# Kernel tuning notes

Measured on AMD Instinct MI355X. Metric: run time of the kernel, lower is better.

Reference implementation:

```python
import jax, jax.numpy as jnp
import numpy as np

K_NN = 10      # knn_graph(landmarks, 10)
K_HOPS = 2     # TAGConv K
DELTA_T = 10
EPS = 0.1


def knn_edges(pos, k=K_NN):
    # PyG knn_graph with loop=False, flow='source_to_target':
    # edges (src=neighbor j, dst=query i), k nearest excluding self.
    n = pos.shape[0]
    sq = jnp.sum(pos * pos, axis=-1)
    d = sq[:, None] + sq[None, :] - 2.0 * (pos @ pos.T)  # [N,N] squared dists
    d = jnp.where(jnp.eye(n, dtype=bool), jnp.inf, d)
    _, idx = jax.lax.top_k(-d, k)                        # [N,k] neighbor ids
    src = idx.reshape(-1)                                # neighbors (sources)
    dst = jnp.repeat(jnp.arange(n), k)                   # query nodes (targets)
    return src, dst


def tagconv(h, src, dst, conv_ws, conv_b):
    # out = sum_{k=0..K} (A_norm^k h) W_k + b, gcn_norm without self-loops
    n = h.shape[0]
    deg = jax.ops.segment_sum(jnp.ones_like(src, dtype=h.dtype), dst, num_segments=n)
    dinv = jnp.where(deg > 0, jax.lax.rsqrt(deg), 0.0)
    norm = dinv[src] * dinv[dst]                         # [E]
    out = h @ conv_ws[0]
    x = h
    for k in range(1, K_HOPS + 1):
        msg = x[src] * norm[:, None]                     # gather + scale [E,D]
        x = jax.ops.segment_sum(msg, dst, num_segments=n)
        out = out + x @ conv_ws[k]
    return out + conv_b


def setup_inputs() -> dict:
    key = jax.random.key(0)
    ks = jax.random.split(key, 7)
    N, D_IN, D_H, D_OUT = 8192, 3, 256, 3
    s_emb = 1.0 / np.sqrt(D_IN)
    s_h = 1.0 / np.sqrt(D_H)
    return {
        "landmarks": jax.random.normal(ks[0], (N, D_IN), jnp.float32),
        "emb_w": jax.random.normal(ks[1], (D_IN, D_H), jnp.float32) * s_emb,
        "emb_b": jax.random.normal(ks[2], (D_H,), jnp.float32) * 0.01,
        "readout_w": jax.random.normal(ks[3], (D_H, D_OUT), jnp.float32) * s_h,
        "readout_b": jax.random.normal(ks[4], (D_OUT,), jnp.float32) * 0.01,
        "conv_ws": jax.random.normal(ks[5], (K_HOPS + 1, D_H, D_H), jnp.float32) * s_h,
        "conv_b": jax.random.normal(ks[6], (D_H,), jnp.float32) * 0.01,
    }


def reference(landmarks, emb_w, emb_b, readout_w, readout_b, conv_ws, conv_b):
    src, dst = knn_edges(landmarks)
    h = landmarks @ emb_w + emb_b                        # emb
    x = h @ readout_w + readout_b                        # readout of initial state

    def step(hc, _):
        c = tagconv(hc, src, dst, conv_ws, conv_b)
        hn = hc + EPS * jnp.tanh(c)                      # Euler residual step
        return hn, hn @ readout_w + readout_b

    h_final, land_pred = jax.lax.scan(step, h, None, length=DELTA_T)
    y = h_final @ readout_w + readout_b
    return y, h_final, x, land_pred
```

## Files before the change

### kernel.cpp

```cpp
#include <hip/hip_runtime.h>
#include <float.h>
#include <math.h>

#define NN 8192
#define DH 256
#define KNN 10
#define TSTEPS 10
#define EPSC 0.1f
#define CTILE 1024
#define QPB 16

typedef short s8v __attribute__((ext_vector_type(8)));
typedef float f4v __attribute__((ext_vector_type(4)));

__device__ __forceinline__ float bf2f(unsigned short u) {
    union { unsigned u; float f; } c; c.u = ((unsigned)u) << 16; return c.f;
}
__device__ __forceinline__ unsigned short f2bf(float f) {
    union { float f; unsigned u; } c; c.f = f;
    unsigned r = c.u + 0x7FFF + ((c.u >> 16) & 1);
    return (unsigned short)(r >> 16);
}

__global__ void prep_wt(const float* __restrict__ W, unsigned short* __restrict__ Wt) {
    int e = blockIdx.x * 256 + threadIdx.x;
    int g = e >> 16; int rem = e & 65535;
    int n = rem >> 8; int k = rem & 255;
    Wt[e] = f2bf(W[g * 65536 + k * 256 + n]);
}

__global__ void prep_pos(const float* __restrict__ pos, float4* __restrict__ pos4) {
    int j = blockIdx.x * 256 + threadIdx.x;
    float x = pos[j * 3], y = pos[j * 3 + 1], z = pos[j * 3 + 2];
    float4 v; v.x = x; v.y = y; v.z = z; v.w = x * x + y * y + z * z;
    pos4[j] = v;
}

__launch_bounds__(1024)
__global__ void knn_wave(const float* __restrict__ pos, const float4* __restrict__ pos4,
                         int* __restrict__ nbr) {
    __shared__ float4 cand[CTILE];
    int tid = threadIdx.x;
    int wv = tid >> 6, lane = tid & 63;
    int i = blockIdx.x * QPB + wv;
    float xi = pos[i * 3], yi = pos[i * 3 + 1], zi = pos[i * 3 + 2];
    float sqi = xi * xi + yi * yi + zi * zi;
    int igrp = i & ~63;

    float b  = FLT_MAX;
    int   ib = -1;
    float thr = FLT_MAX;

    for (int tile = 0; tile < NN / CTILE; ++tile) {
        __syncthreads();
        cand[tid] = pos4[tile * CTILE + tid];
        __syncthreads();
#pragma unroll 4
        for (int u = 0; u < CTILE / 64; ++u) {
            int jgrp = tile * CTILE + u * 64;
            float4 c = cand[u * 64 + lane];
            int j = jgrp + lane;
            float m = c.x * xi + c.y * yi + c.z * zi;
            float d = (sqi + c.w) - 2.0f * m;
            if (jgrp == igrp) {
                if (j == i) d = FLT_MAX;
            }
            unsigned long long mask = __ballot(d < thr);
            while (mask) {
                int l = __ffsll((unsigned long long)mask) - 1;
                mask &= mask - 1;
                float dc = __int_as_float(__builtin_amdgcn_readlane(__float_as_int(d), l));
                if (dc < thr) {
                    int jc = __builtin_amdgcn_readlane(j, l);
                    float bp = __int_as_float(__builtin_amdgcn_update_dpp(
                        0, __float_as_int(b), 0x111, 0xF, 0xF, true));
                    int ip = __builtin_amdgcn_update_dpp(0, ib, 0x111, 0xF, 0xF, true);
                    bool c0 = dc < b;
                    bool cp = (lane != 0) && (dc < bp);
                    b  = c0 ? (cp ? bp : dc) : b;
                    ib = c0 ? (cp ? ip : jc) : ib;
                    thr = __int_as_float(__builtin_amdgcn_readlane(__float_as_int(b), 9));
                }
            }
        }
    }
    if (lane < KNN) nbr[i * KNN + lane] = ib;
}

__global__ void emb_kernel(const float* __restrict__ lm, const float* __restrict__ ew,
                           const float* __restrict__ eb, const float* __restrict__ rw,
                           const float* __restrict__ rb,
                           float* __restrict__ hdo, unsigned short* __restrict__ hbf,
                           float* __restrict__ xout) {
    __shared__ float s0[4], s1[4], s2[4];
    int i = blockIdx.x, d = threadIdx.x;
    float a0 = lm[i * 3], a1 = lm[i * 3 + 1], a2 = lm[i * 3 + 2];
    float h = eb[d] + a0 * ew[d] + a1 * ew[256 + d] + a2 * ew[512 + d];
    hdo[i * 256 + d] = h;
    hbf[i * 256 + d] = f2bf(h);
    float p0 = h * rw[d * 3], p1 = h * rw[d * 3 + 1], p2 = h * rw[d * 3 + 2];
    for (int off = 32; off; off >>= 1) {
        p0 += __shfl_down(p0, off, 64);
        p1 += __shfl_down(p1, off, 64);
        p2 += __shfl_down(p2, off, 64);
    }
    int lane = d & 63, wid = d >> 6;
    if (lane == 0) { s0[wid] = p0; s1[wid] = p1; s2[wid] = p2; }
    __syncthreads();
    if (d == 0) {
        xout[i * 3 + 0] = s0[0] + s0[1] + s0[2] + s0[3] + rb[0];
        xout[i * 3 + 1] = s1[0] + s1[1] + s1[2] + s1[3] + rb[1];
        xout[i * 3 + 2] = s2[0] + s2[1] + s2[2] + s2[3] + rb[2];
    }
}

__global__ void agg_kernel(const unsigned short* __restrict__ src,
                           unsigned short* __restrict__ dst,
                           const int* __restrict__ nbr) {
    int tid = threadIdx.x;
    int wid = tid >> 6, lane = tid & 63;
    int node = blockIdx.x * 4 + wid;
    int d0 = lane * 4;
    float a0 = 0.f, a1 = 0.f, a2 = 0.f, a3 = 0.f;
    const int* nb = nbr + node * KNN;
    for (int q = 0; q < KNN; q++) {
        int j = nb[q];
        uint2 v = *(const uint2*)(src + j * 256 + d0);
        a0 += bf2f((unsigned short)(v.x & 0xffff));
        a1 += bf2f((unsigned short)(v.x >> 16));
        a2 += bf2f((unsigned short)(v.y & 0xffff));
        a3 += bf2f((unsigned short)(v.y >> 16));
    }
    uint2 o;
    o.x = (unsigned)f2bf(a0 * 0.1f) | ((unsigned)f2bf(a1 * 0.1f) << 16);
    o.y = (unsigned)f2bf(a2 * 0.1f) | ((unsigned)f2bf(a3 * 0.1f) << 16);
    *(uint2*)(dst + node * 256 + d0) = o;
}

__launch_bounds__(1024)
__global__ void gemm_step(unsigned short* hbf,
                          const unsigned short* __restrict__ x1,
                          const int* __restrict__ nbr,
                          const unsigned short* __restrict__ Wt,
                          const float* __restrict__ cb,
                          const float* __restrict__ rw, const float* __restrict__ rb,
                          float* hdo, float* __restrict__ yout, float* yfin) {
    __shared__ __align__(16) short Al[32 * 264];
    __shared__ __align__(16) short X2[32 * 264];
    __shared__ __align__(16) short Bl[2][256 * 72];
    __shared__ float rwl[768];
    __shared__ float cbl[256];
    __shared__ float yred[16][4][4][3];

    int tid = threadIdx.x;
    int m0 = blockIdx.x * 32;
    if (tid < 768) rwl[tid] = rw[tid];
    if (tid < 256) cbl[tid] = cb[tid];

    int w = tid >> 6, lane = tid & 63;
    int quad = lane >> 4, l15 = lane & 15;
    int rt = w >> 3, cfg = w & 7;

    int arow = tid >> 5, acg = tid & 31;
    int bn = tid >> 2, bk = (tid & 3) * 16;

    {
        const int* nb = nbr + (m0 + arow) * KNN;
        float a[8];
#pragma unroll
        for (int e = 0; e < 8; e++) a[e] = 0.f;
        for (int q = 0; q < KNN; q++) {
            int j = nb[q];
            uint4 v = *(const uint4*)(x1 + j * 256 + acg * 8);
            a[0] += bf2f((unsigned short)(v.x & 0xffff));
            a[1] += bf2f((unsigned short)(v.x >> 16));
            a[2] += bf2f((unsigned short)(v.y & 0xffff));
            a[3] += bf2f((unsigned short)(v.y >> 16));
            a[4] += bf2f((unsigned short)(v.z & 0xffff));
            a[5] += bf2f((unsigned short)(v.z >> 16));
            a[6] += bf2f((unsigned short)(v.w & 0xffff));
            a[7] += bf2f((unsigned short)(v.w >> 16));
        }
        uint4 o;
        o.x = (unsigned)f2bf(a[0]*0.1f) | ((unsigned)f2bf(a[1]*0.1f) << 16);
        o.y = (unsigned)f2bf(a[2]*0.1f) | ((unsigned)f2bf(a[3]*0.1f) << 16);
        o.z = (unsigned)f2bf(a[4]*0.1f) | ((unsigned)f2bf(a[5]*0.1f) << 16);
        o.w = (unsigned)f2bf(a[6]*0.1f) | ((unsigned)f2bf(a[7]*0.1f) << 16);
        *(uint4*)((unsigned short*)&X2[arow * 264 + acg * 8]) = o;
    }

    {
        uint4 va = *(const uint4*)(((const unsigned short*)hbf) + (m0 + arow) * 256 + acg * 8);
        *(uint4*)((unsigned short*)&Al[arow * 264 + acg * 8]) = va;
        uint4 v0 = *(const uint4*)(Wt + bn * 256 + bk);
        uint4 v1 = *(const uint4*)(Wt + bn * 256 + bk + 8);
        *(uint4*)(&Bl[0][bn * 72 + bk]) = v0;
        *(uint4*)(&Bl[0][bn * 72 + bk + 8]) = v1;
    }
    __syncthreads();

    f4v acc[2];
    acc[0] = (f4v){0.f, 0.f, 0.f, 0.f};
    acc[1] = (f4v){0.f, 0.f, 0.f, 0.f};

#pragma unroll
    for (int kc = 0; kc < 12; kc++) {
        const int cur = kc & 1;
        uint4 v0, v1;
        if (kc + 1 < 12) {
            const unsigned short* bsrc = Wt + ((kc + 1) >> 2) * 65536 + ((kc + 1) & 3) * 64;
            v0 = *(const uint4*)(bsrc + bn * 256 + bk);
            v1 = *(const uint4*)(bsrc + bn * 256 + bk + 8);
        }
        uint4 va;
        if (kc == 3)
            va = *(const uint4*)(x1 + (m0 + arow) * 256 + acg * 8);
        {
            const short* Abase = (kc < 8) ? Al : X2;
            int kl = (kc & 3) * 64;
#pragma unroll
            for (int ks = 0; ks < 2; ks++) {
                s8v a = *(const s8v*)(&Abase[(rt * 16 + l15) * 264 + kl + ks * 32 + quad * 8]);
#pragma unroll
                for (int f = 0; f < 2; f++) {
                    int n = (cfg * 2 + f) * 16 + l15;
                    s8v b = *(const s8v*)(&Bl[cur][n * 72 + ks * 32 + quad * 8]);
                    acc[f] = __builtin_amdgcn_mfma_f32_16x16x32_bf16(a, b, acc[f], 0, 0, 0);
                }
            }
        }
        if (kc + 1 < 12) {
            *(uint4*)(&Bl[cur ^ 1][bn * 72 + bk]) = v0;
            *(uint4*)(&Bl[cur ^ 1][bn * 72 + bk + 8]) = v1;
        }
        __syncthreads();
        if (kc == 3) {
            *(uint4*)((unsigned short*)&Al[arow * 264 + acg * 8]) = va;
            __syncthreads();
        }
    }

    float py[4][3] = {};
#pragma unroll
    for (int f = 0; f < 2; f++) {
        int col = (cfg * 2 + f) * 16 + l15;
        float cbv = cbl[col];
        float rw0 = rwl[col * 3], rw1 = rwl[col * 3 + 1], rw2 = rwl[col * 3 + 2];
#pragma unroll
        for (int r = 0; r < 4; r++) {
            int grow = m0 + rt * 16 + quad * 4 + r;
            float cval = acc[f][r] + cbv;
            float hn = hdo[grow * 256 + col] + EPSC * tanhf(cval);
            hdo[grow * 256 + col] = hn;
            hbf[grow * 256 + col] = f2bf(hn);
            py[r][0] += hn * rw0; py[r][1] += hn * rw1; py[r][2] += hn * rw2;
        }
    }
    for (int off = 1; off < 16; off <<= 1)
        for (int r = 0; r < 4; r++)
            for (int j = 0; j < 3; j++)
                py[r][j] += __shfl_xor(py[r][j], off, 64);
    if (l15 == 0)
        for (int r = 0; r < 4; r++)
            for (int j = 0; j < 3; j++)
                yred[w][quad][r][j] = py[r][j];
    __syncthreads();
    if (w == 0 && l15 == 0) {
        for (int rt2 = 0; rt2 < 2; rt2++) {
            for (int r = 0; r < 4; r++) {
                int grow = m0 + rt2 * 16 + quad * 4 + r;
                for (int j = 0; j < 3; j++) {
                    float yv = rb[j];
                    for (int ww = rt2 * 8; ww < rt2 * 8 + 8; ww++)
                        yv += yred[ww][quad][r][j];
                    yout[grow * 3 + j] = yv;
                    if (yfin) yfin[grow * 3 + j] = yv;
                }
            }
        }
    }
}

extern "C" void kernel_launch(void* const* d_in, const int* in_sizes, int n_in,
                              void* d_out, int out_size, void* d_ws, size_t ws_size,
                              hipStream_t stream) {
    const float* lm = (const float*)d_in[0];
    const float* ew = (const float*)d_in[1];
    const float* eb = (const float*)d_in[2];
    const float* rw = (const float*)d_in[3];
    const float* rb = (const float*)d_in[4];
    const float* cw = (const float*)d_in[5];
    const float* cb = (const float*)d_in[6];

    float* out = (float*)d_out;
    float* y_out = out;
    float* h_out = out + 24576;
    float* x_out = out + 24576 + 2097152;
    float* lp_out = x_out + 24576;

    char* ws = (char*)d_ws;
    int* nbr = (int*)ws;                       ws += NN * KNN * sizeof(int);
    float4* pos4 = (float4*)ws;                ws += NN * sizeof(float4);
    char* uni = ws;
    unsigned short* hbf = (unsigned short*)uni;
    unsigned short* x1  = hbf + NN * DH;
    unsigned short* Wt  = x1 + NN * DH;

    prep_pos<<<NN / 256, 256, 0, stream>>>(lm, pos4);
    knn_wave<<<NN / QPB, 1024, 0, stream>>>(lm, pos4, nbr);
    prep_wt<<<768, 256, 0, stream>>>(cw, Wt);
    emb_kernel<<<NN, 256, 0, stream>>>(lm, ew, eb, rw, rb, h_out, hbf, x_out);
    for (int t = 0; t < TSTEPS; t++) {
        agg_kernel<<<NN / 4, 256, 0, stream>>>(hbf, x1, nbr);
        gemm_step<<<NN / 32, 1024, 0, stream>>>(hbf, x1, nbr, Wt, cb, rw, rb, h_out,
                                                lp_out + t * 24576,
                                                (t == TSTEPS - 1) ? y_out : nullptr);
    }
}
```

Before: 398.8 us.

## Pre-swizzle weights into MFMA fragment layout and drop LDS B staging

Weights are now pre-permuted on the device into the exact per-lane MFMA B-fragment order, so the GEMM reads B fragments straight from global/L2 with no LDS double buffering and no barriers inside the k-loop. The GEMM tile shrinks to 16 rows with 512 threads and a launch bound of 4 blocks per CU, trading B reuse across rows for occupancy and fewer syncs. The aggregation kernel switches to 16-byte loads with all ten neighbour loads issued up front. The main risk is higher L2 traffic for weights, since every block re-reads all 384 KB of Wt.

```diff
diff --git a/kernel.cpp b/kernel.cpp
--- a/kernel.cpp
+++ b/kernel.cpp
@@ -24,8 +24,11 @@
 
 __global__ void prep_wt(const float* __restrict__ W, unsigned short* __restrict__ Wt) {
     int e = blockIdx.x * 256 + threadIdx.x;
-    int g = e >> 16; int rem = e & 65535;
-    int n = rem >> 8; int k = rem & 255;
+    int i8 = e & 7, lane = (e >> 3) & 63, nb = (e >> 9) & 15;
+    int ks = (e >> 13) & 1, kc2 = (e >> 14) & 3, g = e >> 16;
+    int quad = lane >> 4, l15 = lane & 15;
+    int k = kc2 * 64 + ks * 32 + quad * 8 + i8;
+    int n = nb * 16 + l15;
     Wt[e] = f2bf(W[g * 65536 + k * 256 + n]);
 }
 
@@ -118,26 +121,39 @@
                            unsigned short* __restrict__ dst,
                            const int* __restrict__ nbr) {
     int tid = threadIdx.x;
-    int wid = tid >> 6, lane = tid & 63;
-    int node = blockIdx.x * 4 + wid;
-    int d0 = lane * 4;
-    float a0 = 0.f, a1 = 0.f, a2 = 0.f, a3 = 0.f;
+    int slot = tid >> 5, l32 = tid & 31;
+    int node = blockIdx.x * 8 + slot;
+    int d0 = l32 * 8;
     const int* nb = nbr + node * KNN;
+    int j[KNN];
+#pragma unroll
+    for (int q = 0; q < KNN; q++) j[q] = nb[q];
+    uint4 v[KNN];
+#pragma unroll
+    for (int q = 0; q < KNN; q++) v[q] = *(const uint4*)(src + j[q] * 256 + d0);
+    float a[8];
+#pragma unroll
+    for (int e = 0; e < 8; e++) a[e] = 0.f;
+#pragma unroll
     for (int q = 0; q < KNN; q++) {
-        int j = nb[q];
-        uint2 v = *(const uint2*)(src + j * 256 + d0);
-        a0 += bf2f((unsigned short)(v.x & 0xffff));
-        a1 += bf2f((unsigned short)(v.x >> 16));
-        a2 += bf2f((unsigned short)(v.y & 0xffff));
-        a3 += bf2f((unsigned short)(v.y >> 16));
-    }
-    uint2 o;
-    o.x = (unsigned)f2bf(a0 * 0.1f) | ((unsigned)f2bf(a1 * 0.1f) << 16);
-    o.y = (unsigned)f2bf(a2 * 0.1f) | ((unsigned)f2bf(a3 * 0.1f) << 16);
-    *(uint2*)(dst + node * 256 + d0) = o;
-}
-
-__launch_bounds__(1024)
+        a[0] += bf2f((unsigned short)(v[q].x & 0xffff));
+        a[1] += bf2f((unsigned short)(v[q].x >> 16));
+        a[2] += bf2f((unsigned short)(v[q].y & 0xffff));
+        a[3] += bf2f((unsigned short)(v[q].y >> 16));
+        a[4] += bf2f((unsigned short)(v[q].z & 0xffff));
+        a[5] += bf2f((unsigned short)(v[q].z >> 16));
+        a[6] += bf2f((unsigned short)(v[q].w & 0xffff));
+        a[7] += bf2f((unsigned short)(v[q].w >> 16));
+    }
+    uint4 o;
+    o.x = (unsigned)f2bf(a[0]*0.1f) | ((unsigned)f2bf(a[1]*0.1f) << 16);
+    o.y = (unsigned)f2bf(a[2]*0.1f) | ((unsigned)f2bf(a[3]*0.1f) << 16);
+    o.z = (unsigned)f2bf(a[4]*0.1f) | ((unsigned)f2bf(a[5]*0.1f) << 16);
+    o.w = (unsigned)f2bf(a[6]*0.1f) | ((unsigned)f2bf(a[7]*0.1f) << 16);
+    *(uint4*)(dst + node * 256 + d0) = o;
+}
+
+__launch_bounds__(512, 4)
 __global__ void gemm_step(unsigned short* hbf,
                           const unsigned short* __restrict__ x1,
                           const int* __restrict__ nbr,
@@ -145,33 +161,39 @@
                           const float* __restrict__ cb,
                           const float* __restrict__ rw, const float* __restrict__ rb,
                           float* hdo, float* __restrict__ yout, float* yfin) {
-    __shared__ __align__(16) short Al[32 * 264];
-    __shared__ __align__(16) short X2[32 * 264];
-    __shared__ __align__(16) short Bl[2][256 * 72];
+    __shared__ __align__(16) short Ah[16 * 264];
+    __shared__ __align__(16) short A1[16 * 264];
+    __shared__ __align__(16) short X2[16 * 264];
     __shared__ float rwl[768];
     __shared__ float cbl[256];
-    __shared__ float yred[16][4][4][3];
+    __shared__ float yred[8][4][4][3];
 
     int tid = threadIdx.x;
-    int m0 = blockIdx.x * 32;
-    if (tid < 768) rwl[tid] = rw[tid];
+    int m0 = blockIdx.x * 16;
+    for (int idx = tid; idx < 768; idx += 512) rwl[idx] = rw[idx];
     if (tid < 256) cbl[tid] = cb[tid];
 
     int w = tid >> 6, lane = tid & 63;
     int quad = lane >> 4, l15 = lane & 15;
-    int rt = w >> 3, cfg = w & 7;
-
-    int arow = tid >> 5, acg = tid & 31;
-    int bn = tid >> 2, bk = (tid & 3) * 16;
+    int row = tid >> 5, cg = tid & 31;
 
     {
-        const int* nb = nbr + (m0 + arow) * KNN;
+        uint4 va = *(const uint4*)(((const unsigned short*)hbf) + (m0 + row) * 256 + cg * 8);
+        *(uint4*)((unsigned short*)&Ah[row * 264 + cg * 8]) = va;
+        uint4 vb = *(const uint4*)(x1 + (m0 + row) * 256 + cg * 8);
+        *(uint4*)((unsigned short*)&A1[row * 264 + cg * 8]) = vb;
+    }
+    {
+        const int* nb = nbr + (m0 + row) * KNN;
+        int j[KNN];
+#pragma unroll
+        for (int q = 0; q < KNN; q++) j[q] = nb[q];
         float a[8];
 #pragma unroll
         for (int e = 0; e < 8; e++) a[e] = 0.f;
+#pragma unroll
         for (int q = 0; q < KNN; q++) {
-            int j = nb[q];
-            uint4 v = *(const uint4*)(x1 + j * 256 + acg * 8);
+            uint4 v = *(const uint4*)(x1 + j[q] * 256 + cg * 8);
             a[0] += bf2f((unsigned short)(v.x & 0xffff));
             a[1] += bf2f((unsigned short)(v.x >> 16));
             a[2] += bf2f((unsigned short)(v.y & 0xffff));
@@ -186,16 +208,7 @@
         o.y = (unsigned)f2bf(a[2]*0.1f) | ((unsigned)f2bf(a[3]*0.1f) << 16);
         o.z = (unsigned)f2bf(a[4]*0.1f) | ((unsigned)f2bf(a[5]*0.1f) << 16);
         o.w = (unsigned)f2bf(a[6]*0.1f) | ((unsigned)f2bf(a[7]*0.1f) << 16);
-        *(uint4*)((unsigned short*)&X2[arow * 264 + acg * 8]) = o;
-    }
-
-    {
-        uint4 va = *(const uint4*)(((const unsigned short*)hbf) + (m0 + arow) * 256 + acg * 8);
-        *(uint4*)((unsigned short*)&Al[arow * 264 + acg * 8]) = va;
-        uint4 v0 = *(const uint4*)(Wt + bn * 256 + bk);
-        uint4 v1 = *(const uint4*)(Wt + bn * 256 + bk + 8);
-        *(uint4*)(&Bl[0][bn * 72 + bk]) = v0;
-        *(uint4*)(&Bl[0][bn * 72 + bk + 8]) = v1;
+        *(uint4*)((unsigned short*)&X2[row * 264 + cg * 8]) = o;
     }
     __syncthreads();
 
@@ -205,50 +218,28 @@
 
 #pragma unroll
     for (int kc = 0; kc < 12; kc++) {
-        const int cur = kc & 1;
-        uint4 v0, v1;
-        if (kc + 1 < 12) {
-            const unsigned short* bsrc = Wt + ((kc + 1) >> 2) * 65536 + ((kc + 1) & 3) * 64;
-            v0 = *(const uint4*)(bsrc + bn * 256 + bk);
-            v1 = *(const uint4*)(bsrc + bn * 256 + bk + 8);
-        }
-        uint4 va;
-        if (kc == 3)
-            va = *(const uint4*)(x1 + (m0 + arow) * 256 + acg * 8);
-        {
-            const short* Abase = (kc < 8) ? Al : X2;
-            int kl = (kc & 3) * 64;
-#pragma unroll
-            for (int ks = 0; ks < 2; ks++) {
-                s8v a = *(const s8v*)(&Abase[(rt * 16 + l15) * 264 + kl + ks * 32 + quad * 8]);
-#pragma unroll
-                for (int f = 0; f < 2; f++) {
-                    int n = (cfg * 2 + f) * 16 + l15;
-                    s8v b = *(const s8v*)(&Bl[cur][n * 72 + ks * 32 + quad * 8]);
-                    acc[f] = __builtin_amdgcn_mfma_f32_16x16x32_bf16(a, b, acc[f], 0, 0, 0);
-                }
+        const short* Ab = (kc < 4) ? Ah : (kc < 8) ? A1 : X2;
+        int kl = (kc & 3) * 64;
+#pragma unroll
+        for (int ks = 0; ks < 2; ks++) {
+            s8v a = *(const s8v*)(&Ab[l15 * 264 + kl + ks * 32 + quad * 8]);
+#pragma unroll
+            for (int f = 0; f < 2; f++) {
+                s8v b = *(const s8v*)(Wt + ((kc * 2 + ks) * 16 + (w * 2 + f)) * 512 + lane * 8);
+                acc[f] = __builtin_amdgcn_mfma_f32_16x16x32_bf16(a, b, acc[f], 0, 0, 0);
             }
         }
-        if (kc + 1 < 12) {
-            *(uint4*)(&Bl[cur ^ 1][bn * 72 + bk]) = v0;
-            *(uint4*)(&Bl[cur ^ 1][bn * 72 + bk + 8]) = v1;
-        }
-        __syncthreads();
-        if (kc == 3) {
-            *(uint4*)((unsigned short*)&Al[arow * 264 + acg * 8]) = va;
-            __syncthreads();
-        }
     }
 
     float py[4][3] = {};
 #pragma unroll
     for (int f = 0; f < 2; f++) {
-        int col = (cfg * 2 + f) * 16 + l15;
+        int col = w * 32 + f * 16 + l15;
         float cbv = cbl[col];
         float rw0 = rwl[col * 3], rw1 = rwl[col * 3 + 1], rw2 = rwl[col * 3 + 2];
 #pragma unroll
         for (int r = 0; r < 4; r++) {
-            int grow = m0 + rt * 16 + quad * 4 + r;
+            int grow = m0 + quad * 4 + r;
             float cval = acc[f][r] + cbv;
             float hn = hdo[grow * 256 + col] + EPSC * tanhf(cval);
             hdo[grow * 256 + col] = hn;
@@ -266,16 +257,13 @@
                 yred[w][quad][r][j] = py[r][j];
     __syncthreads();
     if (w == 0 && l15 == 0) {
-        for (int rt2 = 0; rt2 < 2; rt2++) {
-            for (int r = 0; r < 4; r++) {
-                int grow = m0 + rt2 * 16 + quad * 4 + r;
-                for (int j = 0; j < 3; j++) {
-                    float yv = rb[j];
-                    for (int ww = rt2 * 8; ww < rt2 * 8 + 8; ww++)
-                        yv += yred[ww][quad][r][j];
-                    yout[grow * 3 + j] = yv;
-                    if (yfin) yfin[grow * 3 + j] = yv;
-                }
+        for (int r = 0; r < 4; r++) {
+            int grow = m0 + quad * 4 + r;
+            for (int j = 0; j < 3; j++) {
+                float yv = rb[j];
+                for (int ww = 0; ww < 8; ww++) yv += yred[ww][quad][r][j];
+                yout[grow * 3 + j] = yv;
+                if (yfin) yfin[grow * 3 + j] = yv;
             }
         }
     }
@@ -311,9 +299,9 @@
     prep_wt<<<768, 256, 0, stream>>>(cw, Wt);
     emb_kernel<<<NN, 256, 0, stream>>>(lm, ew, eb, rw, rb, h_out, hbf, x_out);
     for (int t = 0; t < TSTEPS; t++) {
-        agg_kernel<<<NN / 4, 256, 0, stream>>>(hbf, x1, nbr);
-        gemm_step<<<NN / 32, 1024, 0, stream>>>(hbf, x1, nbr, Wt, cb, rw, rb, h_out,
-                                                lp_out + t * 24576,
-                                                (t == TSTEPS - 1) ? y_out : nullptr);
-    }
-}
+        agg_kernel<<<NN / 8, 256, 0, stream>>>(hbf, x1, nbr);
+        gemm_step<<<NN / 16, 512, 0, stream>>>(hbf, x1, nbr, Wt, cb, rw, rb, h_out,
+                                               lp_out + t * 24576,
+                                               (t == TSTEPS - 1) ? y_out : nullptr);
+    }
+}
```

After: 380.1 us. 1.05x faster.
